# Optimization experiments

Hardware: AMD Instinct MI355X
Metric: run time of the kernel (lower is better)

The kernel has to match this reference:

```python
import jax, jax.numpy as jnp
import numpy as np
import math

B, S, D, H = 2, 2048, 1024, 16
HD = D // H  # 64


def setup_inputs() -> dict:
    key = jax.random.key(0)
    ks = jax.random.split(key, 12)
    s = 1.0 / math.sqrt(D)
    inp = {
        "x": jax.random.normal(ks[0], (B, S, D), dtype=jnp.float32),
        "Wq": jax.random.normal(ks[1], (D, D), dtype=jnp.float32) * s,
        "bq": jnp.zeros((D,), dtype=jnp.float32),
        "Wk": jax.random.normal(ks[2], (D, D), dtype=jnp.float32) * s,
        "bk": jnp.zeros((D,), dtype=jnp.float32),
        "Wv": jax.random.normal(ks[3], (D, D), dtype=jnp.float32) * s,
        "bv": jnp.zeros((D,), dtype=jnp.float32),
        "Wo": jax.random.normal(ks[4], (D, D), dtype=jnp.float32) * s,
        "bo": jnp.zeros((D,), dtype=jnp.float32),
        "cross_modal_weights": jnp.ones((3, 3), dtype=jnp.float32),
        "mask": jax.random.randint(ks[5], (B, S, S), 0, 2, dtype=jnp.int32),
        "modality_info": jax.random.randint(ks[6], (B, S), 0, 3, dtype=jnp.int64),
    }
    return inp


def reference(x, Wq, bq, Wk, bk, Wv, bv, Wo, bo, cross_modal_weights, mask, modality_info):
    b, s, d = x.shape
    # QKV projections -> [b, H, s, HD]
    q = (x @ Wq + bq).reshape(b, s, H, HD).transpose(0, 2, 1, 3)
    k = (x @ Wk + bk).reshape(b, s, H, HD).transpose(0, 2, 1, 3)
    v = (x @ Wv + bv).reshape(b, s, H, HD).transpose(0, 2, 1, 3)
    scores = jnp.einsum("bhqd,bhkd->bhqk", q, k) / math.sqrt(HD)
    # modality bias: torch uses .item() -> detached scalar
    modality_bias = jax.lax.stop_gradient(jnp.mean(cross_modal_weights))
    scores = scores + modality_bias
    # user mask [b, s, s] broadcast over heads; masked_fill(mask==0, -1e9)
    scores = jnp.where(mask[:, None, :, :] == 0, jnp.float32(-1e9), scores)
    attn = jax.nn.softmax(scores, axis=-1)
    # dropout_rate = 0.0 (eval) -> identity
    ctx = jnp.einsum("bhqk,bhkd->bhqd", attn, v)
    ctx = ctx.transpose(0, 2, 1, 3).reshape(b, s, d)
    return ctx @ Wo + bo
```

## Files before the change

kernel.cpp:

```cpp
#include <hip/hip_runtime.h>
#include <math.h>

#define Bdim 2
#define Sdim 2048
#define Ddim 1024
#define Hnum 16
#define HDdim 64
#define Kdim 1024

using short8   = __attribute__((ext_vector_type(8))) short;
using ushort8  = __attribute__((ext_vector_type(8))) unsigned short;
using ushort4v = __attribute__((ext_vector_type(4))) unsigned short;
using floatx4  = __attribute__((ext_vector_type(4))) float;
using half4    = __attribute__((ext_vector_type(4))) _Float16;
using half2v   = __attribute__((ext_vector_type(2))) _Float16;

__device__ __forceinline__ unsigned short f2bf(float f) {
    __bf16 b = (__bf16)f;
    return __builtin_bit_cast(unsigned short, b);
}

__device__ __forceinline__ void async_ld16(const unsigned short* g, unsigned short* l) {
    __builtin_amdgcn_global_load_lds(
        (const __attribute__((address_space(1))) unsigned int*)(g),
        (__attribute__((address_space(3))) unsigned int*)(l), 16, 0, 0);
}

__global__ __launch_bounds__(256) void prep_kernel(
    const float* __restrict__ x,
    const float* __restrict__ Wq, const float* __restrict__ Wk,
    const float* __restrict__ Wv, const float* __restrict__ Wo,
    const int* __restrict__ mask,
    unsigned short* __restrict__ xb, unsigned short* __restrict__ Wt,
    unsigned long long* __restrict__ packed)
{
    __shared__ float tile[64][65];
    const int bid = blockIdx.x;
    const int t   = threadIdx.x;

    if (bid < 2048) {
        size_t i = ((size_t)bid * 256 + t) * 8;
        float4 a = *(const float4*)(x + i);
        float4 b = *(const float4*)(x + i + 4);
        ushort8 o;
        o[0] = f2bf(a.x); o[1] = f2bf(a.y); o[2] = f2bf(a.z); o[3] = f2bf(a.w);
        o[4] = f2bf(b.x); o[5] = f2bf(b.y); o[6] = f2bf(b.z); o[7] = f2bf(b.w);
        *(ushort8*)(xb + i) = o;
    } else if (bid < 3072) {
        const int idx = bid - 2048;
        const int n0 = (idx & 15) * 64;
        const int k0 = ((idx >> 4) & 15) * 64;
        const int z  = idx >> 8;
        const float* W = (z == 0) ? Wq : (z == 1) ? Wk : (z == 2) ? Wv : Wo;
        unsigned short* outp = Wt + (size_t)z * Kdim * Ddim;
#pragma unroll
        for (int i = 0; i < 4; ++i) {
            int flat = i * 256 + t;
            int r = flat >> 4;
            int c = (flat & 15) * 4;
            float4 v = *(const float4*)(W + (size_t)(k0 + r) * Ddim + n0 + c);
            tile[r][c] = v.x; tile[r][c+1] = v.y; tile[r][c+2] = v.z; tile[r][c+3] = v.w;
        }
        __syncthreads();
#pragma unroll
        for (int i = 0; i < 16; ++i) {
            int flat = i * 256 + t;
            int n = flat >> 6;
            int k = flat & 63;
            outp[(size_t)(n0 + n) * Kdim + k0 + k] = f2bf(tile[k][n]);
        }
    } else {
        const int lane = t & 63;
        const int l15  = lane & 15;
        const int quad = lane >> 4;
        const unsigned int gid = (bid - 3072) * 4 + (t >> 6);
        const int b  = gid >> 14;
        const int qg = (gid >> 7) & 127;
        const int kb = gid & 127;
        int4 mv = *(const int4*)(mask + ((size_t)(b * Sdim) + qg * 16 + l15) * Sdim + kb * 16 + quad * 4);
        unsigned long long w0 = __ballot(mv.x != 0);
        unsigned long long w1 = __ballot(mv.y != 0);
        unsigned long long w2 = __ballot(mv.z != 0);
        unsigned long long w3 = __ballot(mv.w != 0);
        if (lane == 0) {
            unsigned long long* dst = packed + (size_t)gid * 4;
            dst[0] = w0; dst[1] = w1; dst[2] = w2; dst[3] = w3;
        }
    }
}

#define MFMA_NORM(MT, NT) acc[MT][NT] = __builtin_amdgcn_mfma_f32_16x16x32_bf16(af[MT], bfr[NT], acc[MT][NT], 0, 0, 0)
#define MFMA_SWAP(MT, NT) acc[MT][NT] = __builtin_amdgcn_mfma_f32_16x16x32_bf16(bfr[NT], af[MT], acc[MT][NT], 0, 0, 0)

#define GEMM_KLOOP(APTR, WPTR, NT_TILES, MFMA_STMT)                              \
    for (int kt = 0; kt < 16; ++kt) {                                            \
        const int k0 = kt * 64;                                                  \
        __syncthreads();                                                         \
        _Pragma("unroll")                                                        \
        for (int i = 0; i < 4; ++i) {                                            \
            int flat = i * 256 + t;                                              \
            int row  = flat >> 3;                                                \
            int cg   = (flat & 7) ^ (row & 7);                                   \
            async_ld16(APTR + (size_t)(m0 + row) * Kdim + k0 + cg * 8,           \
                       As + flat * 8);                                           \
        }                                                                        \
        _Pragma("unroll")                                                        \
        for (int i = 0; i < NT_TILES; ++i) {                                     \
            int flat = i * 256 + t;                                              \
            int row  = flat >> 3;                                                \
            int cg   = (flat & 7) ^ (row & 7);                                   \
            async_ld16(WPTR + (size_t)row * Kdim + k0 + cg * 8,                  \
                       Bs + flat * 8);                                           \
        }                                                                        \
        __syncthreads();                                                         \
        _Pragma("unroll")                                                        \
        for (int ks = 0; ks < 2; ++ks) {                                         \
            short8 af[4], bfr[NT_TILES];                                         \
            _Pragma("unroll")                                                    \
            for (int mt = 0; mt < 4; ++mt) {                                     \
                int row = wm * 64 + mt * 16 + l15;                               \
                int ch  = (ks * 4 + quad) ^ (row & 7);                           \
                af[mt] = *(const short8*)(As + row * 64 + ch * 8);               \
            }                                                                    \
            _Pragma("unroll")                                                    \
            for (int nt = 0; nt < NT_TILES; ++nt) {                              \
                int row = wn * (NT_TILES * 16) + nt * 16 + l15;                  \
                int ch  = (ks * 4 + quad) ^ (row & 7);                           \
                bfr[nt] = *(const short8*)(Bs + row * 64 + ch * 8);              \
            }                                                                    \
            _Pragma("unroll")                                                    \
            for (int mt = 0; mt < 4; ++mt)                                       \
                _Pragma("unroll")                                                \
                for (int nt = 0; nt < NT_TILES; ++nt)                            \
                    MFMA_STMT(mt, nt);                                           \
        }                                                                        \
    }

__global__ __launch_bounds__(256, 4) void qkv_mfma_kernel(
    const unsigned short* __restrict__ A, const unsigned short* __restrict__ Wt,
    const float* __restrict__ bq, const float* __restrict__ bk, const float* __restrict__ bv,
    unsigned short* __restrict__ qo, unsigned short* __restrict__ ko, _Float16* __restrict__ vto)
{
    __shared__ __align__(16) unsigned short As[128 * 64];
    __shared__ __align__(16) unsigned short Bs[128 * 64];
    const int lin = blockIdx.y * 24 + blockIdx.x;
    const int xcd = lin & 7;
    const int idx = lin >> 3;
    const int bx  = (xcd & 1) * 12 + idx % 12;
    const int by  = (xcd >> 1) * 8 + idx / 12;
    const int n0   = bx * 128;
    const int m0   = by * 128;
    const int wsel = n0 >> 10;
    const int c0   = n0 & 1023;
    const unsigned short* Wp = Wt + (size_t)wsel * Kdim * Ddim + (size_t)c0 * Kdim;

    const int t    = threadIdx.x;
    const int lane = t & 63;
    const int w    = t >> 6;
    const int quad = lane >> 4;
    const int l15  = lane & 15;
    const int wm   = w & 1;
    const int wn   = w >> 1;
    floatx4 acc[4][4];
#pragma unroll
    for (int mt = 0; mt < 4; ++mt)
#pragma unroll
        for (int nt = 0; nt < 4; ++nt) acc[mt][nt] = (floatx4){0.f, 0.f, 0.f, 0.f};

    if (wsel < 2) {
        GEMM_KLOOP(A, Wp, 4, MFMA_SWAP)
        const float* bias = wsel ? bk : bq;
        unsigned short* outp = wsel ? ko : qo;
        const float qsc = wsel ? 1.0f : 0.18033688011112042f;
#pragma unroll
        for (int mt = 0; mt < 4; ++mt) {
            int m    = m0 + wm * 64 + mt * 16 + l15;
            int bidx = m >> 11;
            int s    = m & 2047;
#pragma unroll
            for (int nt = 0; nt < 4; ++nt) {
                int c = c0 + wn * 64 + nt * 16 + quad * 4;
                float4 bb = *(const float4*)(bias + c);
                int h  = c >> 6;
                int hd = c & 63;
                ushort4v o;
                o[0] = f2bf((acc[mt][nt][0] + bb.x) * qsc);
                o[1] = f2bf((acc[mt][nt][1] + bb.y) * qsc);
                o[2] = f2bf((acc[mt][nt][2] + bb.z) * qsc);
                o[3] = f2bf((acc[mt][nt][3] + bb.w) * qsc);
                *(ushort4v*)(outp + ((size_t)(bidx * Hnum + h) * Sdim + s) * HDdim + hd) = o;
            }
        }
    } else {
        GEMM_KLOOP(A, Wp, 4, MFMA_NORM)
#pragma unroll
        for (int nt = 0; nt < 4; ++nt) {
            int c = c0 + wn * 64 + nt * 16 + l15;
            float bb = bv[c];
            int h  = c >> 6;
            int hd = c & 63;
#pragma unroll
            for (int mt = 0; mt < 4; ++mt) {
                int m    = m0 + wm * 64 + mt * 16 + quad * 4;
                int bidx = m >> 11;
                int s    = m & 2047;
                half4 o;
#pragma unroll
                for (int r = 0; r < 4; ++r) o[r] = (_Float16)(acc[mt][nt][r] + bb);
                *(half4*)(vto + ((size_t)(bidx * Hnum + h) * HDdim + hd) * Sdim + s) = o;
            }
        }
    }
}

__global__ __launch_bounds__(256, 4) void out_mfma_kernel(
    const unsigned short* __restrict__ A, const unsigned short* __restrict__ Wt,
    const float* __restrict__ bias, float* __restrict__ out)
{
    __shared__ __align__(16) unsigned short As[128 * 64];
    __shared__ __align__(16) unsigned short Bs[64 * 64];
    const int lin = blockIdx.y * 16 + blockIdx.x;
    const int xcd = lin & 7;
    const int idx = lin >> 3;
    const int bx  = idx & 15;
    const int by  = xcd * 4 + (idx >> 4);
    const int n0 = bx * 64;
    const int m0 = by * 128;
    const unsigned short* Wp = Wt + (size_t)3 * Kdim * Ddim + (size_t)n0 * Kdim;

    const int t    = threadIdx.x;
    const int lane = t & 63;
    const int w    = t >> 6;
    const int quad = lane >> 4;
    const int l15  = lane & 15;
    const int wm   = w & 1;
    const int wn   = w >> 1;
    floatx4 acc[4][2];
#pragma unroll
    for (int mt = 0; mt < 4; ++mt)
#pragma unroll
        for (int nt = 0; nt < 2; ++nt) acc[mt][nt] = (floatx4){0.f, 0.f, 0.f, 0.f};

    GEMM_KLOOP(A, Wp, 2, MFMA_SWAP)

#pragma unroll
    for (int mt = 0; mt < 4; ++mt) {
        int m = m0 + wm * 64 + mt * 16 + l15;
#pragma unroll
        for (int nt = 0; nt < 2; ++nt) {
            int c = n0 + wn * 32 + nt * 16 + quad * 4;
            float4 bb = *(const float4*)(bias + c);
            float4 o = make_float4(acc[mt][nt][0] + bb.x, acc[mt][nt][1] + bb.y,
                                   acc[mt][nt][2] + bb.z, acc[mt][nt][3] + bb.w);
            *(float4*)(out + (size_t)m * Ddim + c) = o;
        }
    }
}

__global__ __launch_bounds__(512, 4) void attn_mfma_kernel(
    const unsigned short* __restrict__ q, const unsigned short* __restrict__ k,
    const _Float16* __restrict__ vt, const unsigned long long* __restrict__ pmask,
    unsigned short* __restrict__ ctx)
{
    __shared__ __align__(16) unsigned short Ks[2][64 * 64];
    __shared__ __align__(16) _Float16       Vs[2][64 * 64];
    __shared__ float redl[512];

    const int t    = threadIdx.x;
    const int w    = t >> 6;
    const int lane = t & 63;
    const int quad = lane >> 4;
    const int l15  = lane & 15;
    const int bid  = blockIdx.x;
    const int bh   = bid & 31;
    const int qseg = bid >> 5;
    const int b    = bh >> 4;
    const int h    = bh & 15;
    const int wq   = w & 3;
    const int wk   = w >> 2;
    const int qrow0 = qseg * 128 + wq * 32;

    const unsigned short* qp = q  + (size_t)bh * Sdim * HDdim;
    const unsigned short* kp = k  + (size_t)bh * Sdim * HDdim;
    const _Float16*       vp = vt + (size_t)bh * HDdim * Sdim;

    const int qg0 = __builtin_amdgcn_readfirstlane(qrow0 >> 4);
    const int wku = __builtin_amdgcn_readfirstlane(wk);
    const unsigned long long* __restrict__ pm =
        pmask + ((size_t)(b * 128 + qg0) * 128) * 4 + wku * 8;

    short8 qf[2][2];
#pragma unroll
    for (int g = 0; g < 2; ++g)
#pragma unroll
        for (int ks = 0; ks < 2; ++ks)
            qf[g][ks] = *(const short8*)(qp + (size_t)(qrow0 + g * 16 + l15) * HDdim + ks * 32 + quad * 8);

    floatx4 acc[2][4];
    floatx4 accl[2];
#pragma unroll
    for (int g = 0; g < 2; ++g) {
        accl[g] = (floatx4){0.f, 0.f, 0.f, 0.f};
#pragma unroll
        for (int hs = 0; hs < 4; ++hs) acc[g][hs] = (floatx4){0.f, 0.f, 0.f, 0.f};
    }
    const half4 ones = {(_Float16)1.f, (_Float16)1.f, (_Float16)1.f, (_Float16)1.f};

    auto stage = [&](int buf, int key0) {
        int row = t >> 3;
        int cg  = (t & 7) ^ (row & 7);
        async_ld16(kp + (size_t)(key0 + row) * HDdim + cg * 8, &Ks[buf][t * 8]);
        async_ld16((const unsigned short*)(vp + (size_t)row * Sdim + key0 + cg * 8),
                   (unsigned short*)&Vs[buf][t * 8]);
    };

    stage(0, 0);

#pragma unroll 2
    for (int kt = 0; kt < 32; ++kt) {
        const int cur = kt & 1;
        __syncthreads();
        if (kt < 31) stage(cur ^ 1, (kt + 1) * 64);

        short8 kf[2][2];
#pragma unroll
        for (int ks = 0; ks < 2; ++ks)
#pragma unroll
            for (int sub = 0; sub < 2; ++sub) {
                int row = wk * 32 + sub * 16 + l15;
                int ch  = (ks * 4 + quad) ^ (row & 7);
                kf[ks][sub] = *(const short8*)&Ks[cur][row * 64 + ch * 8];
            }
        half4 vf[4][2];
#pragma unroll
        for (int hs = 0; hs < 4; ++hs)
#pragma unroll
            for (int c = 0; c < 2; ++c) {
                int row = hs * 16 + l15;
                int cc  = (wk * 2 + c) * 2 + (quad >> 1);
                int ch  = cc ^ (row & 7);
                vf[hs][c] = *(const half4*)&Vs[cur][row * 64 + ch * 8 + (quad & 1) * 4];
            }

        floatx4 sc[2][2];
#pragma unroll
        for (int g = 0; g < 2; ++g)
#pragma unroll
            for (int sub = 0; sub < 2; ++sub) sc[g][sub] = (floatx4){0.f, 0.f, 0.f, 0.f};
        __builtin_amdgcn_s_setprio(1);
#pragma unroll
        for (int ks = 0; ks < 2; ++ks)
#pragma unroll
            for (int sub = 0; sub < 2; ++sub)
#pragma unroll
                for (int g = 0; g < 2; ++g)
                    sc[g][sub] = __builtin_amdgcn_mfma_f32_16x16x32_bf16(
                        kf[ks][sub], qf[g][ks], sc[g][sub], 0, 0, 0);
        __builtin_amdgcn_s_setprio(0);

        half4 pf[2][2];
#pragma unroll
        for (int g = 0; g < 2; ++g) {
            const unsigned long long* __restrict__ pg = pm + g * 512 + kt * 16;
#pragma unroll
            for (int c = 0; c < 2; ++c) {
                float pv[4];
#pragma unroll
                for (int r = 0; r < 4; ++r) {
                    float p = exp2f(sc[g][c][r]);
                    unsigned long long wmask = pg[c * 4 + r];
                    asm("v_cndmask_b32 %0, 0, %1, %2" : "=v"(pv[r]) : "v"(p), "s"(wmask));
                }
                half2v lo = __builtin_bit_cast(half2v, __builtin_amdgcn_cvt_pkrtz(pv[0], pv[1]));
                half2v hi = __builtin_bit_cast(half2v, __builtin_amdgcn_cvt_pkrtz(pv[2], pv[3]));
                pf[g][c][0] = lo[0]; pf[g][c][1] = lo[1];
                pf[g][c][2] = hi[0]; pf[g][c][3] = hi[1];
            }
        }

        __builtin_amdgcn_s_setprio(1);
#pragma unroll
        for (int c = 0; c < 2; ++c) {
#pragma unroll
            for (int hs = 0; hs < 4; ++hs)
#pragma unroll
                for (int g = 0; g < 2; ++g)
                    acc[g][hs] = __builtin_amdgcn_mfma_f32_16x16x16f16(
                        vf[hs][c], pf[g][c], acc[g][hs], 0, 0, 0);
#pragma unroll
            for (int g = 0; g < 2; ++g)
                accl[g] = __builtin_amdgcn_mfma_f32_16x16x16f16(
                    ones, pf[g][c], accl[g], 0, 0, 0);
        }
        __builtin_amdgcn_s_setprio(0);
    }

    __syncthreads();
    float* redA = (float*)&Ks[0][0];
    float* redB = (float*)&Vs[0][0];
    if (wk == 1) {
#pragma unroll
        for (int g = 0; g < 2; ++g) {
#pragma unroll
            for (int hs = 0; hs < 4; ++hs) {
                float* dst = (hs < 2) ? redA : redB;
                int slot = ((wq * 2 + g) * 2 + (hs & 1)) * 64 + lane;
                *(floatx4*)&dst[slot * 4] = acc[g][hs];
            }
            redl[(wq * 2 + g) * 64 + lane] = accl[g][0];
        }
    }
    __syncthreads();
    if (wk == 0) {
#pragma unroll
        for (int g = 0; g < 2; ++g) {
            float lsum = accl[g][0] + redl[(wq * 2 + g) * 64 + lane];
            float inv  = 1.0f / fmaxf(lsum, 1e-30f);
            int row = qrow0 + g * 16 + l15;
#pragma unroll
            for (int hs = 0; hs < 4; ++hs) {
                const float* src = (hs < 2) ? redA : redB;
                int slot = ((wq * 2 + g) * 2 + (hs & 1)) * 64 + lane;
                floatx4 o4 = acc[g][hs] + *(const floatx4*)&src[slot * 4];
                ushort4v o;
#pragma unroll
                for (int r = 0; r < 4; ++r) o[r] = f2bf(o4[r] * inv);
                *(ushort4v*)(ctx + (size_t)(b * Sdim + row) * Ddim + h * 64 + hs * 16 + quad * 4) = o;
            }
        }
    }
}

extern "C" void kernel_launch(void* const* d_in, const int* in_sizes, int n_in,
                              void* d_out, int out_size, void* d_ws, size_t ws_size,
                              hipStream_t stream) {
    const float* x   = (const float*)d_in[0];
    const float* Wq  = (const float*)d_in[1];
    const float* bq  = (const float*)d_in[2];
    const float* Wk  = (const float*)d_in[3];
    const float* bk  = (const float*)d_in[4];
    const float* Wv  = (const float*)d_in[5];
    const float* bv  = (const float*)d_in[6];
    const float* Wo  = (const float*)d_in[7];
    const float* bo  = (const float*)d_in[8];
    const int*  mask = (const int*)d_in[10];
    float* out = (float*)d_out;

    char* ws = (char*)d_ws;
    unsigned short* xb  = (unsigned short*)(ws);
    unsigned short* Wt  = (unsigned short*)(ws + (size_t)8  * 1048576);
    unsigned short* qb  = (unsigned short*)(ws + (size_t)16 * 1048576);
    unsigned short* kb  = (unsigned short*)(ws + (size_t)24 * 1048576);
    _Float16*       vtb = (_Float16*)     (ws + (size_t)32 * 1048576);
    unsigned long long* pmk = (unsigned long long*)(ws + (size_t)40 * 1048576);
    unsigned short* ctxb = xb;

    prep_kernel<<<dim3(11264), 256, 0, stream>>>(x, Wq, Wk, Wv, Wo, mask, xb, Wt, pmk);
    qkv_mfma_kernel<<<dim3(24, 32), 256, 0, stream>>>(xb, Wt, bq, bk, bv, qb, kb, vtb);
    attn_mfma_kernel<<<dim3(512), 512, 0, stream>>>(qb, kb, vtb, pmk, ctxb);
    out_mfma_kernel<<<dim3(16, 32), 256, 0, stream>>>(ctxb, Wt, bo, out);
}
```

Baseline: 229.4 us.

## Split attention key tiles across four warps with 64-query blocks

Reorganizes the attention kernel so each block handles 64 query rows instead of 128, with the 8 warps arranged as 2 query groups by 4 key-slices per 64-key tile. The grid doubles to 1024 blocks and launch bounds request higher occupancy. Each warp does half the MFMA work per tile, and a two-stage cross-warp reduction through shared memory merges the four partial accumulators. The goal is more parallelism and latency hiding, paid for with K/V tiles staged twice as often per query and a longer reduction epilogue.

```diff
diff --git a/kernel.cpp b/kernel.cpp
--- a/kernel.cpp
+++ b/kernel.cpp
@@ -257,7 +257,7 @@
     }
 }
 
-__global__ __launch_bounds__(512, 4) void attn_mfma_kernel(
+__global__ __launch_bounds__(512, 8) void attn_mfma_kernel(
     const unsigned short* __restrict__ q, const unsigned short* __restrict__ k,
     const _Float16* __restrict__ vt, const unsigned long long* __restrict__ pmask,
     unsigned short* __restrict__ ctx)
@@ -276,9 +276,9 @@
     const int qseg = bid >> 5;
     const int b    = bh >> 4;
     const int h    = bh & 15;
-    const int wq   = w & 3;
-    const int wk   = w >> 2;
-    const int qrow0 = qseg * 128 + wq * 32;
+    const int wq   = w & 1;
+    const int wk   = w >> 1;
+    const int qrow0 = qseg * 64 + wq * 32;
 
     const unsigned short* qp = q  + (size_t)bh * Sdim * HDdim;
     const unsigned short* kp = k  + (size_t)bh * Sdim * HDdim;
@@ -287,7 +287,7 @@
     const int qg0 = __builtin_amdgcn_readfirstlane(qrow0 >> 4);
     const int wku = __builtin_amdgcn_readfirstlane(wk);
     const unsigned long long* __restrict__ pm =
-        pmask + ((size_t)(b * 128 + qg0) * 128) * 4 + wku * 8;
+        pmask + ((size_t)(b * 128 + qg0) * 128) * 4 + wku * 4;
 
     short8 qf[2][2];
 #pragma unroll
@@ -322,91 +322,104 @@
         __syncthreads();
         if (kt < 31) stage(cur ^ 1, (kt + 1) * 64);
 
-        short8 kf[2][2];
+        short8 kf[2];
+#pragma unroll
+        for (int ks = 0; ks < 2; ++ks) {
+            int row = wk * 16 + l15;
+            int ch  = (ks * 4 + quad) ^ (row & 7);
+            kf[ks] = *(const short8*)&Ks[cur][row * 64 + ch * 8];
+        }
+        half4 vf[4];
+#pragma unroll
+        for (int hs = 0; hs < 4; ++hs) {
+            int row = hs * 16 + l15;
+            int cc  = wk * 2 + (quad >> 1);
+            int ch  = cc ^ (row & 7);
+            vf[hs] = *(const half4*)&Vs[cur][row * 64 + ch * 8 + (quad & 1) * 4];
+        }
+
+        floatx4 sc[2];
+#pragma unroll
+        for (int g = 0; g < 2; ++g) sc[g] = (floatx4){0.f, 0.f, 0.f, 0.f};
+        __builtin_amdgcn_s_setprio(1);
 #pragma unroll
         for (int ks = 0; ks < 2; ++ks)
 #pragma unroll
-            for (int sub = 0; sub < 2; ++sub) {
-                int row = wk * 32 + sub * 16 + l15;
-                int ch  = (ks * 4 + quad) ^ (row & 7);
-                kf[ks][sub] = *(const short8*)&Ks[cur][row * 64 + ch * 8];
+            for (int g = 0; g < 2; ++g)
+                sc[g] = __builtin_amdgcn_mfma_f32_16x16x32_bf16(
+                    kf[ks], qf[g][ks], sc[g], 0, 0, 0);
+        __builtin_amdgcn_s_setprio(0);
+
+        half4 pf[2];
+#pragma unroll
+        for (int g = 0; g < 2; ++g) {
+            const unsigned long long* __restrict__ pg = pm + g * 512 + kt * 16;
+            float pv[4];
+#pragma unroll
+            for (int r = 0; r < 4; ++r) {
+                float p = exp2f(sc[g][r]);
+                unsigned long long wmask = pg[r];
+                asm("v_cndmask_b32 %0, 0, %1, %2" : "=v"(pv[r]) : "v"(p), "s"(wmask));
             }
-        half4 vf[4][2];
+            half2v lo = __builtin_bit_cast(half2v, __builtin_amdgcn_cvt_pkrtz(pv[0], pv[1]));
+            half2v hi = __builtin_bit_cast(half2v, __builtin_amdgcn_cvt_pkrtz(pv[2], pv[3]));
+            pf[g][0] = lo[0]; pf[g][1] = lo[1];
+            pf[g][2] = hi[0]; pf[g][3] = hi[1];
+        }
+
+        __builtin_amdgcn_s_setprio(1);
 #pragma unroll
         for (int hs = 0; hs < 4; ++hs)
 #pragma unroll
-            for (int c = 0; c < 2; ++c) {
-                int row = hs * 16 + l15;
-                int cc  = (wk * 2 + c) * 2 + (quad >> 1);
-                int ch  = cc ^ (row & 7);
-                vf[hs][c] = *(const half4*)&Vs[cur][row * 64 + ch * 8 + (quad & 1) * 4];
-            }
-
-        floatx4 sc[2][2];
+            for (int g = 0; g < 2; ++g)
+                acc[g][hs] = __builtin_amdgcn_mfma_f32_16x16x16f16(
+                    vf[hs], pf[g], acc[g][hs], 0, 0, 0);
 #pragma unroll
         for (int g = 0; g < 2; ++g)
-#pragma unroll
-            for (int sub = 0; sub < 2; ++sub) sc[g][sub] = (floatx4){0.f, 0.f, 0.f, 0.f};
-        __builtin_amdgcn_s_setprio(1);
-#pragma unroll
-        for (int ks = 0; ks < 2; ++ks)
-#pragma unroll
-            for (int sub = 0; sub < 2; ++sub)
-#pragma unroll
-                for (int g = 0; g < 2; ++g)
-                    sc[g][sub] = __builtin_amdgcn_mfma_f32_16x16x32_bf16(
-                        kf[ks][sub], qf[g][ks], sc[g][sub], 0, 0, 0);
-        __builtin_amdgcn_s_setprio(0);
-
-        half4 pf[2][2];
-#pragma unroll
-        for (int g = 0; g < 2; ++g) {
-            const unsigned long long* __restrict__ pg = pm + g * 512 + kt * 16;
-#pragma unroll
-            for (int c = 0; c < 2; ++c) {
-                float pv[4];
-#pragma unroll
-                for (int r = 0; r < 4; ++r) {
-                    float p = exp2f(sc[g][c][r]);
-                    unsigned long long wmask = pg[c * 4 + r];
-                    asm("v_cndmask_b32 %0, 0, %1, %2" : "=v"(pv[r]) : "v"(p), "s"(wmask));
-                }
-                half2v lo = __builtin_bit_cast(half2v, __builtin_amdgcn_cvt_pkrtz(pv[0], pv[1]));
-                half2v hi = __builtin_bit_cast(half2v, __builtin_amdgcn_cvt_pkrtz(pv[2], pv[3]));
-                pf[g][c][0] = lo[0]; pf[g][c][1] = lo[1];
-                pf[g][c][2] = hi[0]; pf[g][c][3] = hi[1];
-            }
-        }
-
-        __builtin_amdgcn_s_setprio(1);
-#pragma unroll
-        for (int c = 0; c < 2; ++c) {
-#pragma unroll
-            for (int hs = 0; hs < 4; ++hs)
-#pragma unroll
-                for (int g = 0; g < 2; ++g)
-                    acc[g][hs] = __builtin_amdgcn_mfma_f32_16x16x16f16(
-                        vf[hs][c], pf[g][c], acc[g][hs], 0, 0, 0);
-#pragma unroll
-            for (int g = 0; g < 2; ++g)
-                accl[g] = __builtin_amdgcn_mfma_f32_16x16x16f16(
-                    ones, pf[g][c], accl[g], 0, 0, 0);
-        }
+            accl[g] = __builtin_amdgcn_mfma_f32_16x16x16f16(
+                ones, pf[g], accl[g], 0, 0, 0);
         __builtin_amdgcn_s_setprio(0);
     }
 
     __syncthreads();
     float* redA = (float*)&Ks[0][0];
     float* redB = (float*)&Vs[0][0];
-    if (wk == 1) {
-#pragma unroll
-        for (int g = 0; g < 2; ++g) {
-#pragma unroll
-            for (int hs = 0; hs < 4; ++hs) {
-                float* dst = (hs < 2) ? redA : redB;
-                int slot = ((wq * 2 + g) * 2 + (hs & 1)) * 64 + lane;
-                *(floatx4*)&dst[slot * 4] = acc[g][hs];
-            }
+    if (wk == 1 || wk == 3) {
+        float* dst   = (wk == 1) ? redA : redB;
+        int    lbase = (wk == 1) ? 0 : 256;
+#pragma unroll
+        for (int g = 0; g < 2; ++g) {
+#pragma unroll
+            for (int hs = 0; hs < 4; ++hs)
+                *(floatx4*)&dst[(((wq * 2 + g) * 4 + hs) * 64 + lane) * 4] = acc[g][hs];
+            redl[lbase + (wq * 2 + g) * 64 + lane] = accl[g][0];
+        }
+    }
+    __syncthreads();
+    if (wk == 0) {
+#pragma unroll
+        for (int g = 0; g < 2; ++g) {
+#pragma unroll
+            for (int hs = 0; hs < 4; ++hs)
+                acc[g][hs] += *(const floatx4*)&redA[(((wq * 2 + g) * 4 + hs) * 64 + lane) * 4];
+            accl[g][0] += redl[(wq * 2 + g) * 64 + lane];
+        }
+    } else if (wk == 2) {
+#pragma unroll
+        for (int g = 0; g < 2; ++g) {
+#pragma unroll
+            for (int hs = 0; hs < 4; ++hs)
+                acc[g][hs] += *(const floatx4*)&redB[(((wq * 2 + g) * 4 + hs) * 64 + lane) * 4];
+            accl[g][0] += redl[256 + (wq * 2 + g) * 64 + lane];
+        }
+    }
+    __syncthreads();
+    if (wk == 2) {
+#pragma unroll
+        for (int g = 0; g < 2; ++g) {
+#pragma unroll
+            for (int hs = 0; hs < 4; ++hs)
+                *(floatx4*)&redA[(((wq * 2 + g) * 4 + hs) * 64 + lane) * 4] = acc[g][hs];
             redl[(wq * 2 + g) * 64 + lane] = accl[g][0];
         }
     }
@@ -419,9 +432,7 @@
             int row = qrow0 + g * 16 + l15;
 #pragma unroll
             for (int hs = 0; hs < 4; ++hs) {
-                const float* src = (hs < 2) ? redA : redB;
-                int slot = ((wq * 2 + g) * 2 + (hs & 1)) * 64 + lane;
-                floatx4 o4 = acc[g][hs] + *(const floatx4*)&src[slot * 4];
+                floatx4 o4 = acc[g][hs] + *(const floatx4*)&redA[(((wq * 2 + g) * 4 + hs) * 64 + lane) * 4];
                 ushort4v o;
 #pragma unroll
                 for (int r = 0; r < 4; ++r) o[r] = f2bf(o4[r] * inv);
@@ -457,6 +468,6 @@
 
     prep_kernel<<<dim3(11264), 256, 0, stream>>>(x, Wq, Wk, Wv, Wo, mask, xb, Wt, pmk);
     qkv_mfma_kernel<<<dim3(24, 32), 256, 0, stream>>>(xb, Wt, bq, bk, bv, qb, kb, vtb);
-    attn_mfma_kernel<<<dim3(512), 512, 0, stream>>>(qb, kb, vtb, pmk, ctxb);
+    attn_mfma_kernel<<<dim3(1024), 512, 0, stream>>>(qb, kb, vtb, pmk, ctxb);
     out_mfma_kernel<<<dim3(16, 32), 256, 0, stream>>>(ctxb, Wt, bo, out);
 }
```

After: 877.5 us. 3.82x slower.
